# Optimization experiments

Hardware: AMD Instinct MI355X
Metric: run time of the kernel (lower is better)

The kernel has to match this reference:

```python
import jax, jax.numpy as jnp
import numpy as np

B, N = 4, 1024                 # images, proposals per image
C_IN, POOL, HID = 256, 7, 1024
NUM_CLASSES = 21               # 20 fg + background (include_bg=False => +1)
FEAT_DIM = C_IN * POOL * POOL  # 12544
IMAGE_H = IMAGE_W = 800.0
STDS = np.array([0.1, 0.1, 0.2, 0.2], np.float32)
SCORE_THRESH = 0.1
NMS_THRESH = 0.5


def setup_inputs():
    key = jax.random.key(0)
    ks = jax.random.split(key, 11)
    props_feature = jax.random.normal(ks[0], (B * N, FEAT_DIM), jnp.float32)
    # well-formed xyxy proposals inside the image
    xy = jax.random.uniform(ks[1], (B, N, 2), minval=0.0, maxval=IMAGE_W - 64.0)
    wh = jax.random.uniform(ks[2], (B, N, 2), minval=8.0, maxval=256.0)
    proposals = jnp.concatenate([xy, jnp.minimum(xy + wh, IMAGE_W)], axis=-1)
    s = 0.02
    return {
        'props_feature': props_feature,
        'proposals': proposals,
        'fc6_w': jax.random.normal(ks[3], (FEAT_DIM, HID), jnp.float32) * s,
        'fc6_b': jnp.zeros((HID,), jnp.float32),
        'fc7_w': jax.random.normal(ks[4], (HID, HID), jnp.float32) * s,
        'fc7_b': jnp.zeros((HID,), jnp.float32),
        'cls_w': jax.random.normal(ks[5], (HID, NUM_CLASSES), jnp.float32) * s,
        'cls_b': jnp.zeros((NUM_CLASSES,), jnp.float32),
        'box_w': jax.random.normal(ks[6], (HID, NUM_CLASSES * 4), jnp.float32) * s,
        'box_b': jnp.zeros((NUM_CLASSES * 4,), jnp.float32),
    }


def _decode(deltas, props):
    # NormalizedProposalDecoder: deltas [...,4] (normalized), props xyxy [...,4]
    d = deltas * jnp.asarray(STDS)  # means are 0
    w = props[..., 2] - props[..., 0]
    h = props[..., 3] - props[..., 1]
    cx = props[..., 0] + 0.5 * w
    cy = props[..., 1] + 0.5 * h
    pcx = d[..., 0] * w + cx
    pcy = d[..., 1] * h + cy
    pw = jnp.exp(d[..., 2]) * w
    ph = jnp.exp(d[..., 3]) * h
    return jnp.stack([pcx - 0.5 * pw, pcy - 0.5 * ph,
                      pcx + 0.5 * pw, pcy + 0.5 * ph], axis=-1)


def _pairwise_iou(a, b):
    lt = jnp.maximum(a[:, None, :2], b[None, :, :2])
    rb = jnp.minimum(a[:, None, 2:], b[None, :, 2:])
    wh = jnp.maximum(rb - lt, 0.0)
    inter = wh[..., 0] * wh[..., 1]
    area_a = (a[:, 2] - a[:, 0]) * (a[:, 3] - a[:, 1])
    area_b = (b[:, 2] - b[:, 0]) * (b[:, 3] - b[:, 1])
    return inter / jnp.maximum(area_a[:, None] + area_b[None, :] - inter, 1e-9)


def _nms_keep(boxes, scores, labels, valid):
    # torchvision batched_nms: per-class via coordinate offset trick
    sc = jnp.where(valid, scores, -1.0)
    order = jnp.argsort(-sc)
    off = labels[order].astype(boxes.dtype)[:, None] * (IMAGE_W + 1.0)
    b = boxes[order] + off
    iou = _pairwise_iou(b, b)  # [N, N]
    idx = jnp.arange(N)

    def body(i, keep):
        sup = (iou[i] > NMS_THRESH) & keep[i] & (idx > i)
        return keep & ~sup

    keep_sorted = jax.lax.fori_loop(0, N, body, valid[order])
    return jnp.zeros(N, bool).at[order].set(keep_sorted)


def reference(props_feature, proposals, fc6_w, fc6_b, fc7_w, fc7_b,
              cls_w, cls_b, box_w, box_b):
    # TwoMLPHead
    x = jax.nn.relu(props_feature @ fc6_w + fc6_b)
    x = jax.nn.relu(x @ fc7_w + fc7_b)
    # FastRCNNPredictor
    scores = jax.nn.softmax(x @ cls_w + cls_b, axis=-1).reshape(B, N, NUM_CLASSES)
    deltas = (x @ box_w + box_b).reshape(B, N, NUM_CLASSES, 4)
    boxes = _decode(deltas, proposals[:, :, None, :])  # [B,N,C,4]
    # drop background column, keep per-box max-score class (scores == max mask)
    sc_fg = scores[..., 1:]
    bx_fg = boxes[:, :, 1:, :]
    best = jnp.argmax(sc_fg, axis=-1)                                  # [B,N]
    sc = jnp.take_along_axis(sc_fg, best[..., None], axis=-1)[..., 0]
    bx = jnp.take_along_axis(bx_fg, best[..., None, None], axis=-2)[..., 0, :]
    labels = best + 1
    # BBoxClipToImageSize
    hi = jnp.asarray([IMAGE_W, IMAGE_H, IMAGE_W, IMAGE_H], bx.dtype)
    bx = jnp.clip(bx, jnp.zeros(4, bx.dtype), hi)
    # BBoxSizeFilter(min=0) + score threshold
    valid = ((bx[..., 2] - bx[..., 0] > 0.0) & (bx[..., 3] - bx[..., 1] > 0.0)
             & (sc > SCORE_THRESH))
    keep = jax.vmap(_nms_keep)(bx, sc, labels, valid)                  # [B,N]
    res = jnp.concatenate([bx, (labels - 1).astype(bx.dtype)[..., None],
                           sc[..., None]], axis=-1)                    # [B,N,6]
    res = jnp.where(keep[..., None], res, 0.0)  # padded in place of ragged lists
    rpn_props = jnp.pad(proposals, ((0, 0), (0, 0), (0, 2)))
    rcnn_props = jnp.pad(bx, ((0, 0), (0, 0), (0, 2)))
    return res, keep, rpn_props, rcnn_props
```

## Files before the change

kernel.cpp:

```cpp
#include <hip/hip_runtime.h>
#include <hip/hip_bf16.h>

#define BATCH 4
#define NPROP 1024
#define HID 1024
#define NUM_CLASSES 21
#define FEAT_DIM 12544
#define NPB (BATCH * NPROP)
#define IMG 800.0f
#define SCORE_THRESH 0.1f
#define NMS_THRESH 0.5f
#define NCOL 112

typedef unsigned short u16;
typedef unsigned int u32;
typedef short s16x8 __attribute__((ext_vector_type(8)));
typedef float f32x4 __attribute__((ext_vector_type(4)));

__device__ __forceinline__ void split2(float x0, float x1, u32& hp, u32& lp) {
    __hip_bfloat162 h2 = __float22bfloat162_rn(make_float2(x0, x1));
    u32 h = *(u32*)&h2;
    float f0 = __uint_as_float(h << 16);
    float f1 = __uint_as_float(h & 0xffff0000u);
    __hip_bfloat162 l2 = __float22bfloat162_rn(make_float2(x0 - f0, x1 - f1));
    hp = h;
    lp = *(u32*)&l2;
}

__global__ __launch_bounds__(256) void transpose_split(
    const float* __restrict__ W, u16* __restrict__ WhT, u16* __restrict__ WlT,
    int K, int N)
{
    __shared__ float tile[32][36];
    const int tid = threadIdx.x;
    const int n0 = blockIdx.x * 32;
    const int k0 = blockIdx.y * 32;
    {
        int i = tid >> 3, j4 = (tid & 7) * 4;
        float4 v = *(const float4*)(W + (size_t)(k0 + i) * N + n0 + j4);
        tile[i][j4] = v.x; tile[i][j4 + 1] = v.y; tile[i][j4 + 2] = v.z; tile[i][j4 + 3] = v.w;
    }
    __syncthreads();
    {
        int i = tid >> 3, j4 = (tid & 7) * 4;
        u32 hp0, lp0, hp1, lp1;
        split2(tile[j4 + 0][i], tile[j4 + 1][i], hp0, lp0);
        split2(tile[j4 + 2][i], tile[j4 + 3][i], hp1, lp1);
        size_t o = (size_t)(n0 + i) * K + k0 + j4;
        *(uint2*)&WhT[o] = make_uint2(hp0, hp1);
        *(uint2*)&WlT[o] = make_uint2(lp0, lp1);
    }
}

__global__ void build_wcat(const float* __restrict__ cls_w, const float* __restrict__ box_w,
                           float* __restrict__ Wcat)
{
    int i = blockIdx.x * 256 + threadIdx.x;
    if (i >= HID * NCOL) return;
    int k = i / NCOL, c = i % NCOL;
    float v = 0.0f;
    if (c < 21) v = cls_w[k * 21 + c];
    else if (c < 105) v = box_w[k * 84 + (c - 21)];
    Wcat[i] = v;
}

__global__ __launch_bounds__(256) void gemm_2ph(
    const float* __restrict__ A, const u16* __restrict__ WhT, const u16* __restrict__ WlT,
    const float* __restrict__ bias, float* __restrict__ Cout,
    int M, int Nn, int K, int KC)
{
    __shared__ u16 sm[2 * 16384];

    const int tid = threadIdx.x;
    const int lane = tid & 63;
    const int wv = tid >> 6;
    const int wr = wv >> 1, wc = wv & 1;

    const int flat = blockIdx.x + (blockIdx.y << 3) + (blockIdx.z << 8);
    const int xcd = flat & 7;
    const int j = flat >> 3;
    const int bxi = j & 7;
    const int yy = (j >> 3) & 3;
    const int bz = j >> 5;
    const int bm = (xcd * 4 + yy) * 128;
    const int bn = bxi * 128;
    const int k0 = bz * KC;
    const int NT = KC / 32;

    const int ar = tid >> 1;
    const int ah = tid & 1;
    const float* aPtr = A + (size_t)(bm + ar) * K + ah * 16;
    const int asw = (ar >> 1) & 3;
    const int ac0 = ((2 * ah) ^ asw) << 3;
    const int ac1 = ((2 * ah + 1) ^ asw) << 3;

    int wrow[2], wlc[2];
#pragma unroll
    for (int i = 0; i < 2; ++i) {
        int c = wv * 2 + i;
        wrow[i] = c * 16 + (lane >> 2);
        wlc[i] = ((lane & 3) ^ ((wrow[i] >> 1) & 3)) * 8;
    }

    const int fr = lane & 15, fq = lane >> 4;
    int ia[4], ib[4];
#pragma unroll
    for (int m = 0; m < 4; ++m) {
        int ra = wr * 64 + m * 16 + fr;
        ia[m] = ra * 32 + ((fq ^ ((ra >> 1) & 3)) << 3);
        int rb = wc * 64 + m * 16 + fr;
        ib[m] = rb * 32 + ((fq ^ ((rb >> 1) & 3)) << 3);
    }

    f32x4 acc[4][4];
#pragma unroll
    for (int m = 0; m < 4; ++m)
#pragma unroll
        for (int n = 0; n < 4; ++n)
            acc[m][n] = (f32x4){0.f, 0.f, 0.f, 0.f};

    auto stage_w = [&](u16* dst, int kk) {
#pragma unroll
        for (int i = 0; i < 2; ++i) {
            const int c = wv * 2 + i;
            const u16* gh = WhT + (size_t)(bn + wrow[i]) * K + kk + wlc[i];
            const u16* gl = WlT + (size_t)(bn + wrow[i]) * K + kk + wlc[i];
            __builtin_amdgcn_global_load_lds(
                (const __attribute__((address_space(1))) u32*)gh,
                (__attribute__((address_space(3))) u32*)(dst + 8192 + c * 512), 16, 0, 0);
            __builtin_amdgcn_global_load_lds(
                (const __attribute__((address_space(1))) u32*)gl,
                (__attribute__((address_space(3))) u32*)(dst + 12288 + c * 512), 16, 0, 0);
        }
    };

    auto split_a = [&](u16* dst, float4 v0, float4 v1, float4 v2, float4 v3) {
        u32 hp[8], lp[8];
        split2(v0.x, v0.y, hp[0], lp[0]);
        split2(v0.z, v0.w, hp[1], lp[1]);
        split2(v1.x, v1.y, hp[2], lp[2]);
        split2(v1.z, v1.w, hp[3], lp[3]);
        split2(v2.x, v2.y, hp[4], lp[4]);
        split2(v2.z, v2.w, hp[5], lp[5]);
        split2(v3.x, v3.y, hp[6], lp[6]);
        split2(v3.z, v3.w, hp[7], lp[7]);
        *(uint4*)&dst[ar * 32 + ac0] = make_uint4(hp[0], hp[1], hp[2], hp[3]);
        *(uint4*)&dst[ar * 32 + ac1] = make_uint4(hp[4], hp[5], hp[6], hp[7]);
        *(uint4*)&dst[4096 + ar * 32 + ac0] = make_uint4(lp[0], lp[1], lp[2], lp[3]);
        *(uint4*)&dst[4096 + ar * 32 + ac1] = make_uint4(lp[4], lp[5], lp[6], lp[7]);
    };

    auto compute = [&](const u16* src) {
        s16x8 fah[4], fal[4], fbh[4], fbl[4];
#pragma unroll
        for (int m = 0; m < 4; ++m) {
            fah[m] = *(const s16x8*)&src[ia[m]];
            fal[m] = *(const s16x8*)&src[4096 + ia[m]];
            fbh[m] = *(const s16x8*)&src[8192 + ib[m]];
            fbl[m] = *(const s16x8*)&src[12288 + ib[m]];
        }
        __builtin_amdgcn_s_setprio(1);
#pragma unroll
        for (int m = 0; m < 4; ++m)
#pragma unroll
            for (int n = 0; n < 4; ++n) {
                acc[m][n] = __builtin_amdgcn_mfma_f32_16x16x32_bf16(fah[m], fbh[n], acc[m][n], 0, 0, 0);
                acc[m][n] = __builtin_amdgcn_mfma_f32_16x16x32_bf16(fah[m], fbl[n], acc[m][n], 0, 0, 0);
                acc[m][n] = __builtin_amdgcn_mfma_f32_16x16x32_bf16(fal[m], fbh[n], acc[m][n], 0, 0, 0);
            }
        __builtin_amdgcn_s_setprio(0);
    };

    u16* bufc = sm;
    u16* bufn = sm + 16384;

    stage_w(bufc, k0);
    {
        float4 a0 = *(const float4*)(aPtr + k0 + 0);
        float4 a1 = *(const float4*)(aPtr + k0 + 4);
        float4 a2 = *(const float4*)(aPtr + k0 + 8);
        float4 a3 = *(const float4*)(aPtr + k0 + 12);
        split_a(bufc, a0, a1, a2, a3);
    }
    asm volatile("s_waitcnt vmcnt(0) lgkmcnt(0)\n\ts_barrier" ::: "memory");

    for (int t = 0; t < NT; ++t) {
        float4 a0{}, a1{}, a2{}, a3{};
        const bool hn = (t + 1 < NT);
        if (hn) {
            const int kk = k0 + (t + 1) * 32;
            stage_w(bufn, kk);
            a0 = *(const float4*)(aPtr + kk + 0);
            a1 = *(const float4*)(aPtr + kk + 4);
            a2 = *(const float4*)(aPtr + kk + 8);
            a3 = *(const float4*)(aPtr + kk + 12);
        }
        compute(bufc);
        if (hn) split_a(bufn, a0, a1, a2, a3);
        asm volatile("s_waitcnt vmcnt(0) lgkmcnt(0)\n\ts_barrier" ::: "memory");
        u16* tmp = bufc; bufc = bufn; bufn = tmp;
    }

    if (bias != nullptr) {
#pragma unroll
        for (int n = 0; n < 4; ++n) {
            int col = bn + wc * 64 + n * 16 + fr;
            float bb = bias[col];
#pragma unroll
            for (int m = 0; m < 4; ++m) {
                int row0 = bm + wr * 64 + m * 16 + fq * 4;
#pragma unroll
                for (int jj = 0; jj < 4; ++jj)
                    Cout[(size_t)(row0 + jj) * Nn + col] = fmaxf(acc[m][n][jj] + bb, 0.0f);
            }
        }
    } else {
        float* Cp = Cout + (size_t)bz * M * Nn;
#pragma unroll
        for (int n = 0; n < 4; ++n) {
            int col = bn + wc * 64 + n * 16 + fr;
#pragma unroll
            for (int m = 0; m < 4; ++m) {
                int row0 = bm + wr * 64 + m * 16 + fq * 4;
#pragma unroll
                for (int jj = 0; jj < 4; ++jj)
                    Cp[(size_t)(row0 + jj) * Nn + col] = acc[m][n][jj];
            }
        }
    }
}

__global__ __launch_bounds__(256) void gemm_split(
    const float* __restrict__ A, const u16* __restrict__ WhT, const u16* __restrict__ WlT,
    const float* __restrict__ bias, float* __restrict__ C, int M, int Nn, int K)
{
    __shared__ u16 sm[4 * 4096];
    u16* sAh = sm;
    u16* sAl = sm + 4096;
    u16* sWh = sm + 8192;
    u16* sWl = sm + 12288;

    const int tid = threadIdx.x;
    const int lane = tid & 63;
    const int wv = tid >> 6;
    const int wr = wv >> 1, wc = wv & 1;
    const int bm = blockIdx.y * 128, bn = blockIdx.x * 128;

    const int ar = tid >> 1;
    const int ah = tid & 1;
    const float* aPtr = A + (size_t)(bm + ar) * K + ah * 16;
    const int asw = (ar >> 1) & 3;
    const int ac0 = ((2 * ah) ^ asw) << 3;
    const int ac1 = ((2 * ah + 1) ^ asw) << 3;

    int wrow[2], wlc[2];
#pragma unroll
    for (int i = 0; i < 2; ++i) {
        int c = wv * 2 + i;
        wrow[i] = c * 16 + (lane >> 2);
        wlc[i] = ((lane & 3) ^ ((wrow[i] >> 1) & 3)) * 8;
    }

    const int fr = lane & 15, fq = lane >> 4;
    int ia[4], ib[4];
#pragma unroll
    for (int m = 0; m < 4; ++m) {
        int ra = wr * 64 + m * 16 + fr;
        ia[m] = ra * 32 + ((fq ^ ((ra >> 1) & 3)) << 3);
        int rb = wc * 64 + m * 16 + fr;
        ib[m] = rb * 32 + ((fq ^ ((rb >> 1) & 3)) << 3);
    }

    f32x4 acc[4][4];
#pragma unroll
    for (int m = 0; m < 4; ++m)
#pragma unroll
        for (int n = 0; n < 4; ++n)
            acc[m][n] = (f32x4){0.f, 0.f, 0.f, 0.f};

    for (int k0 = 0; k0 < K; k0 += 32) {
#pragma unroll
        for (int i = 0; i < 2; ++i) {
            int c = wv * 2 + i;
            const u16* gh = WhT + (size_t)(bn + wrow[i]) * K + k0 + wlc[i];
            const u16* gl = WlT + (size_t)(bn + wrow[i]) * K + k0 + wlc[i];
            __builtin_amdgcn_global_load_lds(
                (const __attribute__((address_space(1))) u32*)gh,
                (__attribute__((address_space(3))) u32*)(sWh + c * 512), 16, 0, 0);
            __builtin_amdgcn_global_load_lds(
                (const __attribute__((address_space(1))) u32*)gl,
                (__attribute__((address_space(3))) u32*)(sWl + c * 512), 16, 0, 0);
        }
        float4 v0 = *(const float4*)(aPtr + k0 + 0);
        float4 v1 = *(const float4*)(aPtr + k0 + 4);
        float4 v2 = *(const float4*)(aPtr + k0 + 8);
        float4 v3 = *(const float4*)(aPtr + k0 + 12);
        u32 hp[8], lp[8];
        split2(v0.x, v0.y, hp[0], lp[0]);
        split2(v0.z, v0.w, hp[1], lp[1]);
        split2(v1.x, v1.y, hp[2], lp[2]);
        split2(v1.z, v1.w, hp[3], lp[3]);
        split2(v2.x, v2.y, hp[4], lp[4]);
        split2(v2.z, v2.w, hp[5], lp[5]);
        split2(v3.x, v3.y, hp[6], lp[6]);
        split2(v3.z, v3.w, hp[7], lp[7]);
        *(uint4*)&sAh[ar * 32 + ac0] = make_uint4(hp[0], hp[1], hp[2], hp[3]);
        *(uint4*)&sAh[ar * 32 + ac1] = make_uint4(hp[4], hp[5], hp[6], hp[7]);
        *(uint4*)&sAl[ar * 32 + ac0] = make_uint4(lp[0], lp[1], lp[2], lp[3]);
        *(uint4*)&sAl[ar * 32 + ac1] = make_uint4(lp[4], lp[5], lp[6], lp[7]);
        __syncthreads();

        s16x8 fah[4], fal[4], fbh[4], fbl[4];
#pragma unroll
        for (int m = 0; m < 4; ++m) {
            fah[m] = *(const s16x8*)&sAh[ia[m]];
            fal[m] = *(const s16x8*)&sAl[ia[m]];
            fbh[m] = *(const s16x8*)&sWh[ib[m]];
            fbl[m] = *(const s16x8*)&sWl[ib[m]];
        }
#pragma unroll
        for (int m = 0; m < 4; ++m)
#pragma unroll
            for (int n = 0; n < 4; ++n) {
                acc[m][n] = __builtin_amdgcn_mfma_f32_16x16x32_bf16(fah[m], fbh[n], acc[m][n], 0, 0, 0);
                acc[m][n] = __builtin_amdgcn_mfma_f32_16x16x32_bf16(fah[m], fbl[n], acc[m][n], 0, 0, 0);
                acc[m][n] = __builtin_amdgcn_mfma_f32_16x16x32_bf16(fal[m], fbh[n], acc[m][n], 0, 0, 0);
            }
        __syncthreads();
    }

#pragma unroll
    for (int n = 0; n < 4; ++n) {
        int col = bn + wc * 64 + n * 16 + fr;
        float bb = bias[col];
#pragma unroll
        for (int m = 0; m < 4; ++m) {
            int row0 = bm + wr * 64 + m * 16 + fq * 4;
#pragma unroll
            for (int jj = 0; jj < 4; ++jj) {
                float v = acc[m][n][jj] + bb;
                C[(size_t)(row0 + jj) * Nn + col] = fmaxf(v, 0.0f);
            }
        }
    }
}

__global__ __launch_bounds__(256) void reduce_bias_relu(
    const float* __restrict__ Cpart, const float* __restrict__ bias,
    float* __restrict__ X, int MN, int Nn)
{
    const int total = MN / 4;
    for (int i4 = blockIdx.x * 256 + threadIdx.x; i4 < total; i4 += gridDim.x * 256) {
        const size_t o = (size_t)i4 * 4;
        float4 a = *(const float4*)(Cpart + o);
        float4 b = *(const float4*)(Cpart + (size_t)MN + o);
        float4 c = *(const float4*)(Cpart + 2 * (size_t)MN + o);
        float4 d = *(const float4*)(Cpart + 3 * (size_t)MN + o);
        float4 bb = *(const float4*)(bias + (o & (size_t)(Nn - 1)));
        float4 r;
        r.x = fmaxf(a.x + b.x + c.x + d.x + bb.x, 0.0f);
        r.y = fmaxf(a.y + b.y + c.y + d.y + bb.y, 0.0f);
        r.z = fmaxf(a.z + b.z + c.z + d.z + bb.z, 0.0f);
        r.w = fmaxf(a.w + b.w + c.w + d.w + bb.w, 0.0f);
        *(float4*)(X + o) = r;
    }
}

__global__ __launch_bounds__(256) void heads_gemm(
    const float* __restrict__ X2, const float* __restrict__ Wcat, float* __restrict__ logits)
{
    __shared__ float Xs[32][36];
    __shared__ float Ws[32 * NCOL];
    const int tid = threadIdx.x;
    const int m0 = blockIdx.x * 32;
    const int tr = tid >> 4;
    const int tc = tid & 15;
    float acc0[7] = {}, acc1[7] = {};
    for (int k0 = 0; k0 < HID; k0 += 32) {
        {
            int i = tid >> 3, j4 = (tid & 7) * 4;
            float4 v = *(const float4*)(X2 + (size_t)(m0 + i) * HID + k0 + j4);
            Xs[i][j4] = v.x; Xs[i][j4 + 1] = v.y; Xs[i][j4 + 2] = v.z; Xs[i][j4 + 3] = v.w;
        }
        const float4* src = (const float4*)(Wcat + (size_t)k0 * NCOL);
        float4* dst = (float4*)Ws;
        for (int i4 = tid; i4 < (32 * NCOL) / 4; i4 += 256) dst[i4] = src[i4];
        __syncthreads();
#pragma unroll 4
        for (int kk = 0; kk < 32; ++kk) {
            float a0 = Xs[tr][kk], a1 = Xs[tr + 16][kk];
#pragma unroll
            for (int j = 0; j < 7; ++j) {
                float b = Ws[kk * NCOL + tc * 7 + j];
                acc0[j] = fmaf(a0, b, acc0[j]);
                acc1[j] = fmaf(a1, b, acc1[j]);
            }
        }
        __syncthreads();
    }
#pragma unroll
    for (int j = 0; j < 7; ++j) {
        logits[(size_t)(m0 + tr) * NCOL + tc * 7 + j] = acc0[j];
        logits[(size_t)(m0 + tr + 16) * NCOL + tc * 7 + j] = acc1[j];
    }
}

__global__ __launch_bounds__(256) void postproc(
    const float* __restrict__ logits, const float* __restrict__ cls_b,
    const float* __restrict__ box_b, const float* __restrict__ proposals,
    float* __restrict__ bxo, float* __restrict__ sco,
    int* __restrict__ lbo, int* __restrict__ vdo)
{
    int p = blockIdx.x * 256 + threadIdx.x;
    if (p >= NPB) return;
    const float* lg = logits + (size_t)p * NCOL;
    float l[21];
    float m = -1e30f;
#pragma unroll
    for (int c = 0; c < 21; ++c) { l[c] = lg[c] + cls_b[c]; m = fmaxf(m, l[c]); }
    float e[21]; float s = 0.0f;
#pragma unroll
    for (int c = 0; c < 21; ++c) { e[c] = expf(l[c] - m); s += e[c]; }
    int best = 1;
#pragma unroll
    for (int c = 2; c < 21; ++c) if (e[c] > e[best]) best = c;
    const float score = e[best] / s;

    float d0 = (lg[21 + best * 4 + 0] + box_b[best * 4 + 0]) * 0.1f;
    float d1 = (lg[21 + best * 4 + 1] + box_b[best * 4 + 1]) * 0.1f;
    float d2 = (lg[21 + best * 4 + 2] + box_b[best * 4 + 2]) * 0.2f;
    float d3 = (lg[21 + best * 4 + 3] + box_b[best * 4 + 3]) * 0.2f;
    const float* pr = proposals + p * 4;
    float w_ = pr[2] - pr[0], h_ = pr[3] - pr[1];
    float cx = pr[0] + 0.5f * w_, cy = pr[1] + 0.5f * h_;
    float pcx = d0 * w_ + cx, pcy = d1 * h_ + cy;
    float pw = expf(d2) * w_, ph = expf(d3) * h_;
    float b0 = pcx - 0.5f * pw, b1 = pcy - 0.5f * ph;
    float b2 = pcx + 0.5f * pw, b3 = pcy + 0.5f * ph;
    b0 = fminf(fmaxf(b0, 0.0f), IMG);
    b1 = fminf(fmaxf(b1, 0.0f), IMG);
    b2 = fminf(fmaxf(b2, 0.0f), IMG);
    b3 = fminf(fmaxf(b3, 0.0f), IMG);
    int vd = (b2 - b0 > 0.0f) && (b3 - b1 > 0.0f) && (score > SCORE_THRESH);
    bxo[p * 4 + 0] = b0; bxo[p * 4 + 1] = b1;
    bxo[p * 4 + 2] = b2; bxo[p * 4 + 3] = b3;
    sco[p] = score;
    lbo[p] = best;
    vdo[p] = vd;
}

__global__ __launch_bounds__(256) void nms_kernel(
    const float* __restrict__ bx, const float* __restrict__ sc,
    const int* __restrict__ label, const int* __restrict__ valid,
    int* __restrict__ keepg)
{
    const int img = blockIdx.x;
    const int base = img * NPROP;
    const int tid = threadIdx.x;
    __shared__ unsigned long long skey[NPROP];
    __shared__ float4 sbx[NPROP];
    __shared__ float sarea[NPROP];
    __shared__ int sord[NPROP];
    __shared__ unsigned char skeep[NPROP];
    __shared__ int nv;

    if (tid == 0) nv = 0;

    for (int i = tid; i < NPROP; i += 256) {
        float s = valid[base + i] ? sc[base + i] : -1.0f;
        unsigned u = __float_as_uint(s);
        u = (u & 0x80000000u) ? ~u : (u | 0x80000000u);
        u = ~u;
        skey[i] = ((unsigned long long)u << 32) | (unsigned)i;
    }
    for (int k = 2; k <= NPROP; k <<= 1) {
        for (int j = k >> 1; j > 0; j >>= 1) {
            __syncthreads();
            for (int i = tid; i < NPROP; i += 256) {
                int ixj = i ^ j;
                if (ixj > i) {
                    unsigned long long a = skey[i], b = skey[ixj];
                    bool up = ((i & k) == 0);
                    if (up ? (a > b) : (a < b)) { skey[i] = b; skey[ixj] = a; }
                }
            }
        }
    }
    __syncthreads();
    for (int r = tid; r < NPROP; r += 256) {
        int p = (int)(skey[r] & 0xffffffffu);
        sord[r] = p;
        float off = (float)label[base + p] * (IMG + 1.0f);
        float x0 = bx[(base + p) * 4 + 0] + off;
        float y0 = bx[(base + p) * 4 + 1] + off;
        float x1 = bx[(base + p) * 4 + 2] + off;
        float y1 = bx[(base + p) * 4 + 3] + off;
        sbx[r] = make_float4(x0, y0, x1, y1);
        sarea[r] = (x1 - x0) * (y1 - y0);
        int v = valid[base + p];
        skeep[r] = (unsigned char)v;
        if (v) atomicMax(&nv, r + 1);
    }
    __syncthreads();
    const int nvalid = nv;

    for (int i = 0; i < nvalid; ++i) {
        if (skeep[i]) {
            float4 bi = sbx[i];
            float ai = sarea[i];
            for (int r = i + 1 + tid; r < nvalid; r += 256) {
                if (skeep[r]) {
                    float4 br_ = sbx[r];
                    float lt0 = fmaxf(bi.x, br_.x);
                    float lt1 = fmaxf(bi.y, br_.y);
                    float rb0 = fminf(bi.z, br_.z);
                    float rb1 = fminf(bi.w, br_.w);
                    float w = fmaxf(rb0 - lt0, 0.0f);
                    float h = fmaxf(rb1 - lt1, 0.0f);
                    float inter = w * h;
                    float denom = fmaxf(ai + sarea[r] - inter, 1e-9f);
                    if (inter / denom > NMS_THRESH) skeep[r] = 0;
                }
            }
        }
        __syncthreads();
    }
    for (int r = tid; r < NPROP; r += 256)
        keepg[base + sord[r]] = skeep[r];
}

__global__ __launch_bounds__(256) void finalize_kernel(
    const float* __restrict__ bx, const float* __restrict__ sc,
    const int* __restrict__ label, const int* __restrict__ keepg,
    const float* __restrict__ proposals, float* __restrict__ out)
{
    const int p = blockIdx.x * blockDim.x + threadIdx.x;
    if (p >= NPB) return;
    float* res = out;
    float* keepo = out + NPB * 6;
    float* rpn = keepo + NPB;
    float* rcnn = rpn + NPB * 6;
    const bool k = keepg[p] != 0;
    float b0 = bx[p * 4 + 0], b1 = bx[p * 4 + 1];
    float b2 = bx[p * 4 + 2], b3 = bx[p * 4 + 3];
    res[p * 6 + 0] = k ? b0 : 0.0f;
    res[p * 6 + 1] = k ? b1 : 0.0f;
    res[p * 6 + 2] = k ? b2 : 0.0f;
    res[p * 6 + 3] = k ? b3 : 0.0f;
    res[p * 6 + 4] = k ? (float)(label[p] - 1) : 0.0f;
    res[p * 6 + 5] = k ? sc[p] : 0.0f;
    keepo[p] = k ? 1.0f : 0.0f;
    rpn[p * 6 + 0] = proposals[p * 4 + 0];
    rpn[p * 6 + 1] = proposals[p * 4 + 1];
    rpn[p * 6 + 2] = proposals[p * 4 + 2];
    rpn[p * 6 + 3] = proposals[p * 4 + 3];
    rpn[p * 6 + 4] = 0.0f;
    rpn[p * 6 + 5] = 0.0f;
    rcnn[p * 6 + 0] = b0;
    rcnn[p * 6 + 1] = b1;
    rcnn[p * 6 + 2] = b2;
    rcnn[p * 6 + 3] = b3;
    rcnn[p * 6 + 4] = 0.0f;
    rcnn[p * 6 + 5] = 0.0f;
}

extern "C" void kernel_launch(void* const* d_in, const int* in_sizes, int n_in,
                              void* d_out, int out_size, void* d_ws, size_t ws_size,
                              hipStream_t stream)
{
    const float* props_feature = (const float*)d_in[0];
    const float* proposals     = (const float*)d_in[1];
    const float* fc6_w         = (const float*)d_in[2];
    const float* fc6_b         = (const float*)d_in[3];
    const float* fc7_w         = (const float*)d_in[4];
    const float* fc7_b         = (const float*)d_in[5];
    const float* cls_w         = (const float*)d_in[6];
    const float* cls_b         = (const float*)d_in[7];
    const float* box_w         = (const float*)d_in[8];
    const float* box_b         = (const float*)d_in[9];
    float* out = (float*)d_out;

    char* ws = (char*)d_ws;
    float* X1     = (float*)(ws);
    float* X2     = (float*)(ws + 16777216);
    float* Wcat   = (float*)(ws + 33554432);
    float* logits = (float*)(ws + 34013184);
    float* bx     = (float*)(ws + 35848192);
    float* sc     = (float*)(ws + 35913728);
    int*   label  = (int*)  (ws + 35930112);
    int*   valid  = (int*)  (ws + 35946496);
    int*   keepg  = (int*)  (ws + 35962880);
    u16*   W6hT   = (u16*)  (ws + 35979264);
    u16*   W6lT   = (u16*)  (ws + 61669376);
    u16*   W7hT   = (u16*)  (ws + 87359488);
    u16*   W7lT   = (u16*)  (ws + 89456640);
    float* Cpart  = (float*)(ws + 91553792);
    const size_t NEED_SK = 91553792ull + 67108864ull;

    transpose_split<<<dim3(HID / 32, FEAT_DIM / 32), 256, 0, stream>>>(
        fc6_w, W6hT, W6lT, FEAT_DIM, HID);
    transpose_split<<<dim3(HID / 32, HID / 32), 256, 0, stream>>>(
        fc7_w, W7hT, W7lT, HID, HID);
    build_wcat<<<(HID * NCOL + 255) / 256, 256, 0, stream>>>(cls_w, box_w, Wcat);

    if (ws_size >= NEED_SK) {
        gemm_2ph<<<dim3(8, 32, 4), 256, 0, stream>>>(
            props_feature, W6hT, W6lT, nullptr, Cpart, NPB, HID, FEAT_DIM, FEAT_DIM / 4);
        reduce_bias_relu<<<1024, 256, 0, stream>>>(Cpart, fc6_b, X1, NPB * HID, HID);
        gemm_2ph<<<dim3(8, 32, 1), 256, 0, stream>>>(
            X1, W7hT, W7lT, fc7_b, X2, NPB, HID, HID, HID);
    } else {
        gemm_split<<<dim3(HID / 128, NPB / 128), 256, 0, stream>>>(
            props_feature, W6hT, W6lT, fc6_b, X1, NPB, HID, FEAT_DIM);
        gemm_split<<<dim3(HID / 128, NPB / 128), 256, 0, stream>>>(
            X1, W7hT, W7lT, fc7_b, X2, NPB, HID, HID);
    }

    heads_gemm<<<NPB / 32, 256, 0, stream>>>(X2, Wcat, logits);
    postproc<<<NPB / 256, 256, 0, stream>>>(logits, cls_b, box_b, proposals,
                                            bx, sc, label, valid);

    nms_kernel<<<BATCH, 256, 0, stream>>>(bx, sc, label, valid, keepg);
    finalize_kernel<<<(NPB + 255) / 256, 256, 0, stream>>>(
        bx, sc, label, keepg, proposals, out);
}
```

Before: 759.9 us.

## Pre-split activations to bf16 hi/lo and stream both operands via LDS DMA

Adds a pre-pass that splits the fc6 input into bf16 high/low arrays once, and makes the fc6 reduction emit split bf16 for fc7. A new double-buffered GEMM then loads both A and W tiles with global_load_lds and raises wave priority around the MFMA block. The aim is to take the per-tile fp32-to-bf16 split and the register-staged A loads off the GEMM inner loop. In exchange it needs a much larger workspace and an extra full pass that reads the 205MB input and writes two half-size copies. If the workspace is too small it falls back to the old path.

```diff
diff --git a/kernel.cpp b/kernel.cpp
--- a/kernel.cpp
+++ b/kernel.cpp
@@ -52,6 +52,23 @@
     }
 }
 
+__global__ __launch_bounds__(256) void split_a_kernel(
+    const float* __restrict__ A, u16* __restrict__ Ah, u16* __restrict__ Al, long n8)
+{
+    for (long i = blockIdx.x * 256L + threadIdx.x; i < n8; i += (long)gridDim.x * 256L) {
+        size_t o = (size_t)i * 8;
+        float4 v0 = *(const float4*)(A + o);
+        float4 v1 = *(const float4*)(A + o + 4);
+        u32 hp[4], lp[4];
+        split2(v0.x, v0.y, hp[0], lp[0]);
+        split2(v0.z, v0.w, hp[1], lp[1]);
+        split2(v1.x, v1.y, hp[2], lp[2]);
+        split2(v1.z, v1.w, hp[3], lp[3]);
+        *(uint4*)&Ah[o] = make_uint4(hp[0], hp[1], hp[2], hp[3]);
+        *(uint4*)&Al[o] = make_uint4(lp[0], lp[1], lp[2], lp[3]);
+    }
+}
+
 __global__ void build_wcat(const float* __restrict__ cls_w, const float* __restrict__ box_w,
                            float* __restrict__ Wcat)
 {
@@ -62,6 +79,143 @@
     if (c < 21) v = cls_w[k * 21 + c];
     else if (c < 105) v = box_w[k * 84 + (c - 21)];
     Wcat[i] = v;
+}
+
+__global__ __launch_bounds__(256) void gemm_2ph_pre(
+    const u16* __restrict__ Ah, const u16* __restrict__ Al,
+    const u16* __restrict__ WhT, const u16* __restrict__ WlT,
+    const float* __restrict__ bias, float* __restrict__ Cout,
+    int M, int Nn, int K, int KC)
+{
+    __shared__ u16 sm[2 * 16384];
+
+    const int tid = threadIdx.x;
+    const int lane = tid & 63;
+    const int wv = tid >> 6;
+    const int wr = wv >> 1, wc = wv & 1;
+
+    const int flat = blockIdx.x + (blockIdx.y << 3) + (blockIdx.z << 8);
+    const int xcd = flat & 7;
+    const int j = flat >> 3;
+    const int bxi = j & 7;
+    const int yy = (j >> 3) & 3;
+    const int bz = j >> 5;
+    const int bm = (xcd * 4 + yy) * 128;
+    const int bn = bxi * 128;
+    const int k0 = bz * KC;
+    const int NT = KC / 32;
+
+    int srow[2], scol[2];
+#pragma unroll
+    for (int i = 0; i < 2; ++i) {
+        int c = wv * 2 + i;
+        srow[i] = c * 16 + (lane >> 2);
+        scol[i] = ((lane & 3) ^ ((srow[i] >> 1) & 3)) * 8;
+    }
+
+    const int fr = lane & 15, fq = lane >> 4;
+    int ia[4], ib[4];
+#pragma unroll
+    for (int m = 0; m < 4; ++m) {
+        int ra = wr * 64 + m * 16 + fr;
+        ia[m] = ra * 32 + ((fq ^ ((ra >> 1) & 3)) << 3);
+        int rb = wc * 64 + m * 16 + fr;
+        ib[m] = rb * 32 + ((fq ^ ((rb >> 1) & 3)) << 3);
+    }
+
+    f32x4 acc[4][4];
+#pragma unroll
+    for (int m = 0; m < 4; ++m)
+#pragma unroll
+        for (int n = 0; n < 4; ++n)
+            acc[m][n] = (f32x4){0.f, 0.f, 0.f, 0.f};
+
+    auto stage = [&](u16* dst, int kk) {
+#pragma unroll
+        for (int i = 0; i < 2; ++i) {
+            const int c = wv * 2 + i;
+            const size_t ao = (size_t)(bm + srow[i]) * K + kk + scol[i];
+            const size_t wo = (size_t)(bn + srow[i]) * K + kk + scol[i];
+            __builtin_amdgcn_global_load_lds(
+                (const __attribute__((address_space(1))) u32*)(Ah + ao),
+                (__attribute__((address_space(3))) u32*)(dst + c * 512), 16, 0, 0);
+            __builtin_amdgcn_global_load_lds(
+                (const __attribute__((address_space(1))) u32*)(Al + ao),
+                (__attribute__((address_space(3))) u32*)(dst + 4096 + c * 512), 16, 0, 0);
+            __builtin_amdgcn_global_load_lds(
+                (const __attribute__((address_space(1))) u32*)(WhT + wo),
+                (__attribute__((address_space(3))) u32*)(dst + 8192 + c * 512), 16, 0, 0);
+            __builtin_amdgcn_global_load_lds(
+                (const __attribute__((address_space(1))) u32*)(WlT + wo),
+                (__attribute__((address_space(3))) u32*)(dst + 12288 + c * 512), 16, 0, 0);
+        }
+    };
+
+    auto compute = [&](const u16* src) {
+        s16x8 fah[4], fal[4], fbh[4], fbl[4];
+#pragma unroll
+        for (int m = 0; m < 4; ++m) {
+            fah[m] = *(const s16x8*)&src[ia[m]];
+            fal[m] = *(const s16x8*)&src[4096 + ia[m]];
+            fbh[m] = *(const s16x8*)&src[8192 + ib[m]];
+            fbl[m] = *(const s16x8*)&src[12288 + ib[m]];
+        }
+        __builtin_amdgcn_s_setprio(1);
+#pragma unroll
+        for (int m = 0; m < 4; ++m)
+#pragma unroll
+            for (int n = 0; n < 4; ++n) {
+                acc[m][n] = __builtin_amdgcn_mfma_f32_16x16x32_bf16(fah[m], fbh[n], acc[m][n], 0, 0, 0);
+                acc[m][n] = __builtin_amdgcn_mfma_f32_16x16x32_bf16(fah[m], fbl[n], acc[m][n], 0, 0, 0);
+                acc[m][n] = __builtin_amdgcn_mfma_f32_16x16x32_bf16(fal[m], fbh[n], acc[m][n], 0, 0, 0);
+            }
+        __builtin_amdgcn_s_setprio(0);
+    };
+
+    u16* bufc = sm;
+    u16* bufn = sm + 16384;
+
+    stage(bufc, k0);
+    for (int t = 0; t < NT; ++t) {
+        if (t + 1 < NT) {
+            stage(bufn, k0 + (t + 1) * 32);
+            asm volatile("s_waitcnt vmcnt(8)" ::: "memory");
+        } else {
+            asm volatile("s_waitcnt vmcnt(0)" ::: "memory");
+        }
+        asm volatile("s_barrier" ::: "memory");
+        compute(bufc);
+        asm volatile("s_barrier" ::: "memory");
+        u16* tmp = bufc; bufc = bufn; bufn = tmp;
+    }
+
+    if (bias != nullptr) {
+#pragma unroll
+        for (int n = 0; n < 4; ++n) {
+            int col = bn + wc * 64 + n * 16 + fr;
+            float bb = bias[col];
+#pragma unroll
+            for (int m = 0; m < 4; ++m) {
+                int row0 = bm + wr * 64 + m * 16 + fq * 4;
+#pragma unroll
+                for (int jj = 0; jj < 4; ++jj)
+                    Cout[(size_t)(row0 + jj) * Nn + col] = fmaxf(acc[m][n][jj] + bb, 0.0f);
+            }
+        }
+    } else {
+        float* Cp = Cout + (size_t)bz * M * Nn;
+#pragma unroll
+        for (int n = 0; n < 4; ++n) {
+            int col = bn + wc * 64 + n * 16 + fr;
+#pragma unroll
+            for (int m = 0; m < 4; ++m) {
+                int row0 = bm + wr * 64 + m * 16 + fq * 4;
+#pragma unroll
+                for (int jj = 0; jj < 4; ++jj)
+                    Cp[(size_t)(row0 + jj) * Nn + col] = acc[m][n][jj];
+            }
+        }
+    }
 }
 
 __global__ __launch_bounds__(256) void gemm_2ph(
@@ -230,121 +384,6 @@
     }
 }
 
-__global__ __launch_bounds__(256) void gemm_split(
-    const float* __restrict__ A, const u16* __restrict__ WhT, const u16* __restrict__ WlT,
-    const float* __restrict__ bias, float* __restrict__ C, int M, int Nn, int K)
-{
-    __shared__ u16 sm[4 * 4096];
-    u16* sAh = sm;
-    u16* sAl = sm + 4096;
-    u16* sWh = sm + 8192;
-    u16* sWl = sm + 12288;
-
-    const int tid = threadIdx.x;
-    const int lane = tid & 63;
-    const int wv = tid >> 6;
-    const int wr = wv >> 1, wc = wv & 1;
-    const int bm = blockIdx.y * 128, bn = blockIdx.x * 128;
-
-    const int ar = tid >> 1;
-    const int ah = tid & 1;
-    const float* aPtr = A + (size_t)(bm + ar) * K + ah * 16;
-    const int asw = (ar >> 1) & 3;
-    const int ac0 = ((2 * ah) ^ asw) << 3;
-    const int ac1 = ((2 * ah + 1) ^ asw) << 3;
-
-    int wrow[2], wlc[2];
-#pragma unroll
-    for (int i = 0; i < 2; ++i) {
-        int c = wv * 2 + i;
-        wrow[i] = c * 16 + (lane >> 2);
-        wlc[i] = ((lane & 3) ^ ((wrow[i] >> 1) & 3)) * 8;
-    }
-
-    const int fr = lane & 15, fq = lane >> 4;
-    int ia[4], ib[4];
-#pragma unroll
-    for (int m = 0; m < 4; ++m) {
-        int ra = wr * 64 + m * 16 + fr;
-        ia[m] = ra * 32 + ((fq ^ ((ra >> 1) & 3)) << 3);
-        int rb = wc * 64 + m * 16 + fr;
-        ib[m] = rb * 32 + ((fq ^ ((rb >> 1) & 3)) << 3);
-    }
-
-    f32x4 acc[4][4];
-#pragma unroll
-    for (int m = 0; m < 4; ++m)
-#pragma unroll
-        for (int n = 0; n < 4; ++n)
-            acc[m][n] = (f32x4){0.f, 0.f, 0.f, 0.f};
-
-    for (int k0 = 0; k0 < K; k0 += 32) {
-#pragma unroll
-        for (int i = 0; i < 2; ++i) {
-            int c = wv * 2 + i;
-            const u16* gh = WhT + (size_t)(bn + wrow[i]) * K + k0 + wlc[i];
-            const u16* gl = WlT + (size_t)(bn + wrow[i]) * K + k0 + wlc[i];
-            __builtin_amdgcn_global_load_lds(
-                (const __attribute__((address_space(1))) u32*)gh,
-                (__attribute__((address_space(3))) u32*)(sWh + c * 512), 16, 0, 0);
-            __builtin_amdgcn_global_load_lds(
-                (const __attribute__((address_space(1))) u32*)gl,
-                (__attribute__((address_space(3))) u32*)(sWl + c * 512), 16, 0, 0);
-        }
-        float4 v0 = *(const float4*)(aPtr + k0 + 0);
-        float4 v1 = *(const float4*)(aPtr + k0 + 4);
-        float4 v2 = *(const float4*)(aPtr + k0 + 8);
-        float4 v3 = *(const float4*)(aPtr + k0 + 12);
-        u32 hp[8], lp[8];
-        split2(v0.x, v0.y, hp[0], lp[0]);
-        split2(v0.z, v0.w, hp[1], lp[1]);
-        split2(v1.x, v1.y, hp[2], lp[2]);
-        split2(v1.z, v1.w, hp[3], lp[3]);
-        split2(v2.x, v2.y, hp[4], lp[4]);
-        split2(v2.z, v2.w, hp[5], lp[5]);
-        split2(v3.x, v3.y, hp[6], lp[6]);
-        split2(v3.z, v3.w, hp[7], lp[7]);
-        *(uint4*)&sAh[ar * 32 + ac0] = make_uint4(hp[0], hp[1], hp[2], hp[3]);
-        *(uint4*)&sAh[ar * 32 + ac1] = make_uint4(hp[4], hp[5], hp[6], hp[7]);
-        *(uint4*)&sAl[ar * 32 + ac0] = make_uint4(lp[0], lp[1], lp[2], lp[3]);
-        *(uint4*)&sAl[ar * 32 + ac1] = make_uint4(lp[4], lp[5], lp[6], lp[7]);
-        __syncthreads();
-
-        s16x8 fah[4], fal[4], fbh[4], fbl[4];
-#pragma unroll
-        for (int m = 0; m < 4; ++m) {
-            fah[m] = *(const s16x8*)&sAh[ia[m]];
-            fal[m] = *(const s16x8*)&sAl[ia[m]];
-            fbh[m] = *(const s16x8*)&sWh[ib[m]];
-            fbl[m] = *(const s16x8*)&sWl[ib[m]];
-        }
-#pragma unroll
-        for (int m = 0; m < 4; ++m)
-#pragma unroll
-            for (int n = 0; n < 4; ++n) {
-                acc[m][n] = __builtin_amdgcn_mfma_f32_16x16x32_bf16(fah[m], fbh[n], acc[m][n], 0, 0, 0);
-                acc[m][n] = __builtin_amdgcn_mfma_f32_16x16x32_bf16(fah[m], fbl[n], acc[m][n], 0, 0, 0);
-                acc[m][n] = __builtin_amdgcn_mfma_f32_16x16x32_bf16(fal[m], fbh[n], acc[m][n], 0, 0, 0);
-            }
-        __syncthreads();
-    }
-
-#pragma unroll
-    for (int n = 0; n < 4; ++n) {
-        int col = bn + wc * 64 + n * 16 + fr;
-        float bb = bias[col];
-#pragma unroll
-        for (int m = 0; m < 4; ++m) {
-            int row0 = bm + wr * 64 + m * 16 + fq * 4;
-#pragma unroll
-            for (int jj = 0; jj < 4; ++jj) {
-                float v = acc[m][n][jj] + bb;
-                C[(size_t)(row0 + jj) * Nn + col] = fmaxf(v, 0.0f);
-            }
-        }
-    }
-}
-
 __global__ __launch_bounds__(256) void reduce_bias_relu(
     const float* __restrict__ Cpart, const float* __restrict__ bias,
     float* __restrict__ X, int MN, int Nn)
@@ -365,6 +404,32 @@
         *(float4*)(X + o) = r;
     }
 }
+
+__global__ __launch_bounds__(256) void reduce_bias_relu_split(
+    const float* __restrict__ Cpart, const float* __restrict__ bias,
+    u16* __restrict__ Xh, u16* __restrict__ Xl, int MN, int Nn)
+{
+    const int total = MN / 4;
+    for (int i4 = blockIdx.x * 256 + threadIdx.x; i4 < total; i4 += gridDim.x * 256) {
+        const size_t o = (size_t)i4 * 4;
+        float4 a = *(const float4*)(Cpart + o);
+        float4 b = *(const float4*)(Cpart + (size_t)MN + o);
+        float4 c = *(const float4*)(Cpart + 2 * (size_t)MN + o);
+        float4 d = *(const float4*)(Cpart + 3 * (size_t)MN + o);
+        float4 bb = *(const float4*)(bias + (o & (size_t)(Nn - 1)));
+        float4 r;
+        r.x = fmaxf(a.x + b.x + c.x + d.x + bb.x, 0.0f);
+        r.y = fmaxf(a.y + b.y + c.y + d.y + bb.y, 0.0f);
+        r.z = fmaxf(a.z + b.z + c.z + d.z + bb.z, 0.0f);
+        r.w = fmaxf(a.w + b.w + c.w + d.w + bb.w, 0.0f);
+        u32 hp[2], lp[2];
+        split2(r.x, r.y, hp[0], lp[0]);
+        split2(r.z, r.w, hp[1], lp[1]);
+        *(uint2*)&Xh[o] = make_uint2(hp[0], hp[1]);
+        *(uint2*)&Xl[o] = make_uint2(lp[0], lp[1]);
+    }
+}
+
 
 __global__ __launch_bounds__(256) void heads_gemm(
     const float* __restrict__ X2, const float* __restrict__ Wcat, float* __restrict__ logits)
@@ -595,7 +660,12 @@
     u16*   W7hT   = (u16*)  (ws + 87359488);
     u16*   W7lT   = (u16*)  (ws + 89456640);
     float* Cpart  = (float*)(ws + 91553792);
-    const size_t NEED_SK = 91553792ull + 67108864ull;
+    u16*   A6h    = (u16*)  (ws + 158662656);
+    u16*   A6l    = (u16*)  (ws + 261423104);
+    u16*   X1h    = (u16*)  (ws + 364183552);
+    u16*   X1l    = (u16*)  (ws + 372572160);
+    const size_t NEED_SK   = 158662656ull;
+    const size_t NEED_FULL = 380960768ull;
 
     transpose_split<<<dim3(HID / 32, FEAT_DIM / 32), 256, 0, stream>>>(
         fc6_w, W6hT, W6lT, FEAT_DIM, HID);
@@ -603,17 +673,26 @@
         fc7_w, W7hT, W7lT, HID, HID);
     build_wcat<<<(HID * NCOL + 255) / 256, 256, 0, stream>>>(cls_w, box_w, Wcat);
 
-    if (ws_size >= NEED_SK) {
+    if (ws_size >= NEED_FULL) {
+        split_a_kernel<<<2048, 256, 0, stream>>>(
+            props_feature, A6h, A6l, (long)NPB * FEAT_DIM / 8);
+        gemm_2ph_pre<<<dim3(8, 32, 4), 256, 0, stream>>>(
+            A6h, A6l, W6hT, W6lT, nullptr, Cpart, NPB, HID, FEAT_DIM, FEAT_DIM / 4);
+        reduce_bias_relu_split<<<1024, 256, 0, stream>>>(
+            Cpart, fc6_b, X1h, X1l, NPB * HID, HID);
+        gemm_2ph_pre<<<dim3(8, 32, 1), 256, 0, stream>>>(
+            X1h, X1l, W7hT, W7lT, fc7_b, X2, NPB, HID, HID, HID);
+    } else if (ws_size >= NEED_SK) {
         gemm_2ph<<<dim3(8, 32, 4), 256, 0, stream>>>(
             props_feature, W6hT, W6lT, nullptr, Cpart, NPB, HID, FEAT_DIM, FEAT_DIM / 4);
         reduce_bias_relu<<<1024, 256, 0, stream>>>(Cpart, fc6_b, X1, NPB * HID, HID);
         gemm_2ph<<<dim3(8, 32, 1), 256, 0, stream>>>(
             X1, W7hT, W7lT, fc7_b, X2, NPB, HID, HID, HID);
     } else {
-        gemm_split<<<dim3(HID / 128, NPB / 128), 256, 0, stream>>>(
-            props_feature, W6hT, W6lT, fc6_b, X1, NPB, HID, FEAT_DIM);
-        gemm_split<<<dim3(HID / 128, NPB / 128), 256, 0, stream>>>(
-            X1, W7hT, W7lT, fc7_b, X2, NPB, HID, HID);
+        gemm_2ph<<<dim3(8, 32, 1), 256, 0, stream>>>(
+            props_feature, W6hT, W6lT, fc6_b, X1, NPB, HID, FEAT_DIM, FEAT_DIM);
+        gemm_2ph<<<dim3(8, 32, 1), 256, 0, stream>>>(
+            X1, W7hT, W7lT, fc7_b, X2, NPB, HID, HID, HID);
     }
 
     heads_gemm<<<NPB / 32, 256, 0, stream>>>(X2, Wcat, logits);
```

New measurement: 820.5 us. +8.0%, slower.
